# Kernel optimization log

Hardware: AMD Instinct MI355X
Metric: run time of the kernel (lower is better)

Reference implementation:

```python
import jax, jax.numpy as jnp
import numpy as np

# Larq ste_sign: forward sign(x) with sign(0)=+1; backward is identity clipped to |x|<=1 (STE).
@jax.custom_vjp
def ste_sign(x):
    return jnp.where(x >= 0, jnp.ones((), x.dtype), -jnp.ones((), x.dtype))

def _ste_fwd(x):
    return ste_sign(x), x

def _ste_bwd(x, g):
    return (g * (jnp.abs(x) <= 1).astype(g.dtype),)

ste_sign.defvjp(_ste_fwd, _ste_bwd)


def setup_inputs() -> dict:
    key = jax.random.key(0)
    k1, k2 = jax.random.split(key)
    x = jax.random.normal(k1, (16, 112, 112, 256), dtype=jnp.float32)      # NHWC
    kernel = jax.random.normal(k2, (3, 3, 256, 1), dtype=jnp.float32) * 0.1  # (kh, kw, C, mult)
    return {"x": x, "kernel": kernel}


def reference(x, kernel):
    # Quantize input and depthwise kernel, then standard depthwise conv (stride 1, SAME, no bias).
    xq = ste_sign(x)
    kq = ste_sign(kernel)
    kh, kw, C, mult = kernel.shape
    rhs = kq.reshape(kh, kw, 1, C * mult)  # HWIO layout for grouped conv
    out = jax.lax.conv_general_dilated(
        xq, rhs,
        window_strides=(1, 1),
        padding="SAME",
        feature_group_count=C,
        dimension_numbers=("NHWC", "HWIO", "NHWC"),
    )
    return out
```

## Files before the change

### kernel.cpp

```cpp
#include <hip/hip_runtime.h>


constexpr int N = 16, H = 112, W = 112, C = 256;
constexpr int TW = 8;
constexpr int R  = 4;

typedef float f32x4 __attribute__((ext_vector_type(4)));

struct TrueT  { static constexpr bool value = true;  };
struct FalseT { static constexpr bool value = false; };

template<bool TOP, bool BOT>
__device__ __forceinline__ void run_tile(
        const float* __restrict__ x, const float* __restrict__ k,
        float* __restrict__ out, int n, int h0, int w0, int c0) {

    unsigned kj3[3][4] = {{0,0,0,0},{0,0,0,0},{0,0,0,0}};
#pragma unroll
    for (int t = 0; t < 9; ++t) {
        const uint4 kv = *reinterpret_cast<const uint4*>(k + t * C + c0);
        const int kr = t / 3, kj = t % 3;
        kj3[kj][0] |= (kv.x >> 31) << kr;
        kj3[kj][1] |= (kv.y >> 31) << kr;
        kj3[kj][2] |= (kv.z >> 31) << kr;
        kj3[kj][3] |= (kv.w >> 31) << kr;
    }

    constexpr int PLO = TOP ? 1 : 0;
    constexpr int PHI = BOT ? R : R + 1;

    const size_t rowstride = (size_t)W * C;
    const float* xin = x + (size_t)(n * H + (h0 - 1)) * rowstride + c0;
    float* o0 = out + (size_t)(n * H + h0) * rowstride + c0;

    auto colSig = [&](int cc, unsigned rs[4]) {
        rs[0] = rs[1] = rs[2] = rs[3] = 0u;
        const float* cp = xin + (size_t)cc * C;
#pragma unroll
        for (int p = PLO; p <= PHI; ++p) {
            const uint4 v = *reinterpret_cast<const uint4*>(cp + (size_t)p * rowstride);
            rs[0] |= (v.x >> 31) << p;
            rs[1] |= (v.y >> 31) << p;
            rs[2] |= (v.z >> 31) << p;
            rs[3] |= (v.w >> 31) << p;
        }
    };

    auto emit = [&](int w, const unsigned rs0[4], const unsigned rs1[4],
                    const unsigned rs2[4], auto h0t, auto h2t) {
#pragma unroll
        for (int r = 0; r < R; ++r) {
            constexpr_if_workaround:;
            const bool border = (TOP && r == 0) || (BOT && r == R - 1);
            const unsigned msk = (TOP && r == 0) ? 0x6u
                               : (BOT && r == R - 1) ? 0x3u : 0x7u;
            const int nr = border ? 2 : 3;
            f32x4 ov;
#pragma unroll
            for (int ch = 0; ch < 4; ++ch) {
                int cnt = 0, nt = 0;
                if constexpr (decltype(h0t)::value) {
                    cnt += __popc(((rs0[ch] >> r) ^ kj3[0][ch]) & msk); nt += nr;
                }
                cnt += __popc(((rs1[ch] >> r) ^ kj3[1][ch]) & msk); nt += nr;
                if constexpr (decltype(h2t)::value) {
                    cnt += __popc(((rs2[ch] >> r) ^ kj3[2][ch]) & msk); nt += nr;
                }
                ov[ch] = (float)(nt - 2 * cnt);
            }
            __builtin_nontemporal_store(ov,
                reinterpret_cast<f32x4*>(o0 + (size_t)r * rowstride + (size_t)w * C));
        }
    };

    unsigned rs_m2[4], rs_m1[4], rs_c[4];

    if (w0 > 0) colSig(w0 - 1, rs_m2);
    else        { rs_m2[0] = rs_m2[1] = rs_m2[2] = rs_m2[3] = 0u; }
    colSig(w0, rs_m1);

    colSig(w0 + 1, rs_c);
    if (w0 > 0) emit(w0, rs_m2, rs_m1, rs_c, TrueT{},  TrueT{});
    else        emit(w0, rs_m2, rs_m1, rs_c, FalseT{}, TrueT{});
#pragma unroll
    for (int ch = 0; ch < 4; ++ch) { rs_m2[ch] = rs_m1[ch]; rs_m1[ch] = rs_c[ch]; }

#pragma unroll 3
    for (int i = 2; i < TW; ++i) {
        colSig(w0 + i, rs_c);
        emit(w0 + i - 1, rs_m2, rs_m1, rs_c, TrueT{}, TrueT{});
#pragma unroll
        for (int ch = 0; ch < 4; ++ch) { rs_m2[ch] = rs_m1[ch]; rs_m1[ch] = rs_c[ch]; }
    }

    if (w0 + TW < W) {
        colSig(w0 + TW, rs_c);
        emit(w0 + TW - 1, rs_m2, rs_m1, rs_c, TrueT{}, TrueT{});
    } else {
        emit(w0 + TW - 1, rs_m2, rs_m1, rs_c, TrueT{}, FalseT{});
    }
}

__global__ __launch_bounds__(256) void bsign_dw3x3_r4(
        const float* __restrict__ x, const float* __restrict__ k,
        float* __restrict__ out) {
    const int c0 = (threadIdx.x & 63) << 2;
    const int wq = threadIdx.x >> 6;
    const int h0 = blockIdx.y * (4 * R) + wq * R;
    const int w0 = blockIdx.x * TW;
    const int n  = blockIdx.z;

    if (h0 == 0)           run_tile<true,  false>(x, k, out, n, h0, w0, c0);
    else if (h0 == H - R)  run_tile<false, true >(x, k, out, n, h0, w0, c0);
    else                   run_tile<false, false>(x, k, out, n, h0, w0, c0);
}

extern "C" void kernel_launch(void* const* d_in, const int* in_sizes, int n_in,
                              void* d_out, int out_size, void* d_ws, size_t ws_size,
                              hipStream_t stream) {
    const float* x = (const float*)d_in[0];
    const float* k = (const float*)d_in[1];
    float* out = (float*)d_out;

    dim3 grid(W / TW, H / (4 * R), N);
    bsign_dw3x3_r4<<<grid, 256, 0, stream>>>(x, k, out);
}
```

Measured before the change: 362.2 us.

## Share per-column sign bitmasks across waves via LDS to cut halo reloads

Each block now loads a 16-row by 16-column input region once, packs the signs into per-column bitmasks in shared memory, and lets all four waves read them after a barrier. Tile width grows from 8 to 14 columns. This removes the redundant global reads of vertical and horizontal halos across waves. The cost is an LDS round-trip, a __syncthreads, and fewer independent blocks, which can reduce latency hiding.

```diff
diff --git a/kernel.cpp b/kernel.cpp
--- a/kernel.cpp
+++ b/kernel.cpp
@@ -2,117 +2,134 @@
 
 
 constexpr int N = 16, H = 112, W = 112, C = 256;
-constexpr int TW = 8;
-constexpr int R  = 4;
+constexpr int TW = 14;
+constexpr int COLS = TW + 2;
+constexpr int RW = 4;
 
 typedef float f32x4 __attribute__((ext_vector_type(4)));
 
 struct TrueT  { static constexpr bool value = true;  };
 struct FalseT { static constexpr bool value = false; };
 
-template<bool TOP, bool BOT>
-__device__ __forceinline__ void run_tile(
+__global__ __launch_bounds__(256, 4) void bsign_dw3x3_lds(
         const float* __restrict__ x, const float* __restrict__ k,
-        float* __restrict__ out, int n, int h0, int w0, int c0) {
+        float* __restrict__ out) {
+    __shared__ unsigned sig[COLS * C];
 
-    unsigned kj3[3][4] = {{0,0,0,0},{0,0,0,0},{0,0,0,0}};
+    const int lane = threadIdx.x & 63;
+    const int wq   = threadIdx.x >> 6;
+    const int c0   = lane << 2;
+    const int h0   = blockIdx.y * 16;
+    const int w0   = blockIdx.x * TW;
+    const int n    = blockIdx.z;
+
+    unsigned k3[3][4] = {{0,0,0,0},{0,0,0,0},{0,0,0,0}};
 #pragma unroll
     for (int t = 0; t < 9; ++t) {
         const uint4 kv = *reinterpret_cast<const uint4*>(k + t * C + c0);
         const int kr = t / 3, kj = t % 3;
-        kj3[kj][0] |= (kv.x >> 31) << kr;
-        kj3[kj][1] |= (kv.y >> 31) << kr;
-        kj3[kj][2] |= (kv.z >> 31) << kr;
-        kj3[kj][3] |= (kv.w >> 31) << kr;
+        k3[kj][0] |= (kv.x >> 31) << kr;
+        k3[kj][1] |= (kv.y >> 31) << kr;
+        k3[kj][2] |= (kv.z >> 31) << kr;
+        k3[kj][3] |= (kv.w >> 31) << kr;
     }
 
-    constexpr int PLO = TOP ? 1 : 0;
-    constexpr int PHI = BOT ? R : R + 1;
+    const size_t rowstride = (size_t)W * C;
 
-    const size_t rowstride = (size_t)W * C;
-    const float* xin = x + (size_t)(n * H + (h0 - 1)) * rowstride + c0;
-    float* o0 = out + (size_t)(n * H + h0) * rowstride + c0;
+    const bool ptop = (h0 > 0);
+    const bool pbot = (h0 + 16 < H);
+#pragma unroll
+    for (int q = 0; q < 4; ++q) {
+        const int ci   = (wq << 2) + q;
+        const int xcol = w0 - 1 + ci;
+        unsigned s0 = 0, s1 = 0, s2 = 0, s3 = 0;
+        if (xcol >= 0 && xcol < W) {
+            const float* cp = x + (size_t)(n * H + h0 - 1) * rowstride
+                                + (size_t)xcol * C + c0;
+#pragma unroll
+            for (int p = 0; p < 18; ++p) {
+                if (p == 0  && !ptop) continue;
+                if (p == 17 && !pbot) continue;
+                const uint4 v = *reinterpret_cast<const uint4*>(
+                    cp + (size_t)p * rowstride);
+                s0 |= (v.x >> 31) << p;
+                s1 |= (v.y >> 31) << p;
+                s2 |= (v.z >> 31) << p;
+                s3 |= (v.w >> 31) << p;
+            }
+        }
+        uint4 sv; sv.x = s0; sv.y = s1; sv.z = s2; sv.w = s3;
+        *reinterpret_cast<uint4*>(&sig[ci * C + c0]) = sv;
+    }
+    __syncthreads();
 
-    auto colSig = [&](int cc, unsigned rs[4]) {
-        rs[0] = rs[1] = rs[2] = rs[3] = 0u;
-        const float* cp = xin + (size_t)cc * C;
+    const int hbase = h0 + (wq << 2);
+    unsigned bm[RW]; int nrr[RW];
 #pragma unroll
-        for (int p = PLO; p <= PHI; ++p) {
-            const uint4 v = *reinterpret_cast<const uint4*>(cp + (size_t)p * rowstride);
-            rs[0] |= (v.x >> 31) << p;
-            rs[1] |= (v.y >> 31) << p;
-            rs[2] |= (v.z >> 31) << p;
-            rs[3] |= (v.w >> 31) << p;
+    for (int r = 0; r < RW; ++r) {
+        const int h = hbase + r;
+        unsigned b = 7u;
+        if (h == 0)     b &= ~1u;
+        if (h == H - 1) b &= ~4u;
+        bm[r]  = b;
+        nrr[r] = (b == 7u) ? 3 : 2;
+    }
+    const int sh0 = wq << 2;
+    float* obase = out + (size_t)(n * H + hbase) * rowstride
+                       + (size_t)w0 * C + c0;
+
+    unsigned m2[4], m1[4], cc[4];
+    auto ldsig = [&](int ci, unsigned d[4]) {
+        const uint4 v = *reinterpret_cast<const uint4*>(&sig[ci * C + c0]);
+        d[0] = v.x >> sh0; d[1] = v.y >> sh0;
+        d[2] = v.z >> sh0; d[3] = v.w >> sh0;
+    };
+    auto emit = [&](int wo, const unsigned a[4], const unsigned bc[4],
+                    const unsigned ce[4], auto jt0, auto jt2) {
+        constexpr int NT = (decltype(jt0)::value ? 1 : 0) + 1
+                         + (decltype(jt2)::value ? 1 : 0);
+        float* orow = obase + (size_t)wo * C;
+#pragma unroll
+        for (int r = 0; r < RW; ++r) {
+            const unsigned b = bm[r];
+            int n0 = 0, n1 = 0, n2 = 0, n3 = 0;
+            auto term = [&](const unsigned s[4], const unsigned kk[4]) {
+                n0 += __popc(((s[0] >> r) ^ kk[0]) & b);
+                n1 += __popc(((s[1] >> r) ^ kk[1]) & b);
+                n2 += __popc(((s[2] >> r) ^ kk[2]) & b);
+                n3 += __popc(((s[3] >> r) ^ kk[3]) & b);
+            };
+            if constexpr (decltype(jt0)::value) term(a, k3[0]);
+            term(bc, k3[1]);
+            if constexpr (decltype(jt2)::value) term(ce, k3[2]);
+            const int nt = NT * nrr[r];
+            f32x4 ov;
+            ov[0] = (float)(nt - 2 * n0);
+            ov[1] = (float)(nt - 2 * n1);
+            ov[2] = (float)(nt - 2 * n2);
+            ov[3] = (float)(nt - 2 * n3);
+            __builtin_nontemporal_store(ov,
+                reinterpret_cast<f32x4*>(orow + (size_t)r * rowstride));
         }
     };
 
-    auto emit = [&](int w, const unsigned rs0[4], const unsigned rs1[4],
-                    const unsigned rs2[4], auto h0t, auto h2t) {
+    ldsig(0, m2); ldsig(1, m1); ldsig(2, cc);
+    if (w0 > 0) emit(0, m2, m1, cc, TrueT{},  TrueT{});
+    else        emit(0, m2, m1, cc, FalseT{}, TrueT{});
 #pragma unroll
-        for (int r = 0; r < R; ++r) {
-            constexpr_if_workaround:;
-            const bool border = (TOP && r == 0) || (BOT && r == R - 1);
-            const unsigned msk = (TOP && r == 0) ? 0x6u
-                               : (BOT && r == R - 1) ? 0x3u : 0x7u;
-            const int nr = border ? 2 : 3;
-            f32x4 ov;
+    for (int ch = 0; ch < 4; ++ch) { m2[ch] = m1[ch]; m1[ch] = cc[ch]; }
+
 #pragma unroll
-            for (int ch = 0; ch < 4; ++ch) {
-                int cnt = 0, nt = 0;
-                if constexpr (decltype(h0t)::value) {
-                    cnt += __popc(((rs0[ch] >> r) ^ kj3[0][ch]) & msk); nt += nr;
-                }
-                cnt += __popc(((rs1[ch] >> r) ^ kj3[1][ch]) & msk); nt += nr;
-                if constexpr (decltype(h2t)::value) {
-                    cnt += __popc(((rs2[ch] >> r) ^ kj3[2][ch]) & msk); nt += nr;
-                }
-                ov[ch] = (float)(nt - 2 * cnt);
-            }
-            __builtin_nontemporal_store(ov,
-                reinterpret_cast<f32x4*>(o0 + (size_t)r * rowstride + (size_t)w * C));
-        }
-    };
-
-    unsigned rs_m2[4], rs_m1[4], rs_c[4];
-
-    if (w0 > 0) colSig(w0 - 1, rs_m2);
-    else        { rs_m2[0] = rs_m2[1] = rs_m2[2] = rs_m2[3] = 0u; }
-    colSig(w0, rs_m1);
-
-    colSig(w0 + 1, rs_c);
-    if (w0 > 0) emit(w0, rs_m2, rs_m1, rs_c, TrueT{},  TrueT{});
-    else        emit(w0, rs_m2, rs_m1, rs_c, FalseT{}, TrueT{});
+    for (int wo = 1; wo < TW - 1; ++wo) {
+        ldsig(wo + 2, cc);
+        emit(wo, m2, m1, cc, TrueT{}, TrueT{});
 #pragma unroll
-    for (int ch = 0; ch < 4; ++ch) { rs_m2[ch] = rs_m1[ch]; rs_m1[ch] = rs_c[ch]; }
-
-#pragma unroll 3
-    for (int i = 2; i < TW; ++i) {
-        colSig(w0 + i, rs_c);
-        emit(w0 + i - 1, rs_m2, rs_m1, rs_c, TrueT{}, TrueT{});
-#pragma unroll
-        for (int ch = 0; ch < 4; ++ch) { rs_m2[ch] = rs_m1[ch]; rs_m1[ch] = rs_c[ch]; }
+        for (int ch = 0; ch < 4; ++ch) { m2[ch] = m1[ch]; m1[ch] = cc[ch]; }
     }
 
-    if (w0 + TW < W) {
-        colSig(w0 + TW, rs_c);
-        emit(w0 + TW - 1, rs_m2, rs_m1, rs_c, TrueT{}, TrueT{});
-    } else {
-        emit(w0 + TW - 1, rs_m2, rs_m1, rs_c, TrueT{}, FalseT{});
-    }
-}
-
-__global__ __launch_bounds__(256) void bsign_dw3x3_r4(
-        const float* __restrict__ x, const float* __restrict__ k,
-        float* __restrict__ out) {
-    const int c0 = (threadIdx.x & 63) << 2;
-    const int wq = threadIdx.x >> 6;
-    const int h0 = blockIdx.y * (4 * R) + wq * R;
-    const int w0 = blockIdx.x * TW;
-    const int n  = blockIdx.z;
-
-    if (h0 == 0)           run_tile<true,  false>(x, k, out, n, h0, w0, c0);
-    else if (h0 == H - R)  run_tile<false, true >(x, k, out, n, h0, w0, c0);
-    else                   run_tile<false, false>(x, k, out, n, h0, w0, c0);
+    ldsig(TW + 1, cc);
+    if (w0 + TW < W) emit(TW - 1, m2, m1, cc, TrueT{}, TrueT{});
+    else             emit(TW - 1, m2, m1, cc, TrueT{}, FalseT{});
 }
 
 extern "C" void kernel_launch(void* const* d_in, const int* in_sizes, int n_in,
@@ -122,6 +139,6 @@
     const float* k = (const float*)d_in[1];
     float* out = (float*)d_out;
 
-    dim3 grid(W / TW, H / (4 * R), N);
-    bsign_dw3x3_r4<<<grid, 256, 0, stream>>>(x, k, out);
+    dim3 grid(W / TW, H / 16, N);
+    bsign_dw3x3_lds<<<grid, 256, 0, stream>>>(x, k, out);
 }
```

Measured after the change: 359.3 us. No clear change (-0.8%).
